# Kernel tuning notes

Hardware: AMD Instinct MI355X
Metric: run time of the kernel (lower is better)

Reference implementation:

```python
import jax, jax.numpy as jnp
import numpy as np

EMBED = 1024
HEADS = 16
HEAD_DIM = EMBED // HEADS
B, S = 2, 2048


def setup_inputs() -> dict:
    key = jax.random.key(0)
    ks = jax.random.split(key, 13)
    def lin(kw, kb):
        # torch nn.Linear default init: U(-1/sqrt(fan_in), 1/sqrt(fan_in))
        bound = 1.0 / np.sqrt(EMBED)
        W = jax.random.uniform(kw, (EMBED, EMBED), jnp.float32, -bound, bound)
        b = jax.random.uniform(kb, (EMBED,), jnp.float32, -bound, bound)
        return W, b
    Wq, bq = lin(ks[0], ks[1])
    Wk, bk = lin(ks[2], ks[3])
    Wv, bv = lin(ks[4], ks[5])
    Wo, bo = lin(ks[6], ks[7])
    return {
        "query": jax.random.normal(ks[8], (B, S, EMBED), jnp.float32),
        "key": jax.random.normal(ks[9], (B, S, EMBED), jnp.float32),
        "value": jax.random.normal(ks[10], (B, S, EMBED), jnp.float32),
        "mask": jax.random.randint(ks[11], (B, S, S), 0, 2, jnp.int32),
        "Wq": Wq, "bq": bq, "Wk": Wk, "bk": bk,
        "Wv": Wv, "bv": bv, "Wo": Wo, "bo": bo,
    }


def _split_heads(x):
    b, s, _ = x.shape
    return x.reshape(b, s, HEADS, HEAD_DIM).transpose(0, 2, 1, 3)  # [B,H,S,D]


def reference(query, key, value, mask, Wq, bq, Wk, bk, Wv, bv, Wo, bo):
    scaling = HEAD_DIM ** -0.5
    q = _split_heads(query @ Wq.T + bq) * scaling          # [B,H,Sq,D]
    k = _split_heads(key @ Wk.T + bk)                       # [B,H,Sk,D]
    v = _split_heads(value @ Wv.T + bv)                     # [B,H,Sk,D]
    scores = jnp.einsum('bhqd,bhkd->bhqk', q, k)            # [B,H,Sq,Sk]
    scores = jnp.where(mask[:, None, :, :] == 0, jnp.float32(-10000.0), scores)
    p = jax.nn.softmax(scores, axis=-1)
    x = jnp.einsum('bhqk,bhkd->bhqd', p, v)                 # [B,H,Sq,D]
    b, h, s, d = x.shape
    x = x.transpose(0, 2, 1, 3).reshape(b, s, h * d)
    return x @ Wo.T + bo
```

## Files before the change

kernel.cpp:

```cpp
#include <hip/hip_runtime.h>

#define EMBED 1024
#define HEADS 16
#define HDIM  64
#define BATCH 2
#define SEQ   2048
#define MTOT  (BATCH*SEQ)
#define LOG2E 1.4426950408889634f
#define QSCALE (0.125f * LOG2E)

typedef __attribute__((ext_vector_type(8)))  short short8;
typedef __attribute__((ext_vector_type(4)))  float f32x4;
typedef __attribute__((ext_vector_type(16))) float f32x16;

#define MFMA(a,b,c)   __builtin_amdgcn_mfma_f32_16x16x32_bf16(a,b,c,0,0,0)
#define MFMA32(a,b,c) __builtin_amdgcn_mfma_f32_32x32x16_bf16(a,b,c,0,0,0)

__device__ __forceinline__ ushort f2bf(float f) {
  union { float f; unsigned u; } v; v.f = f;
  unsigned u = v.u;
  unsigned r = u + 0x7fffu + ((u >> 16) & 1u);
  return (ushort)(r >> 16);
}
__device__ __forceinline__ unsigned packbf(float a, float b) {
  return (unsigned)f2bf(a) | ((unsigned)f2bf(b) << 16);
}
__device__ __forceinline__ unsigned cvtpk(float lo, float hi) {
  unsigned r;
  asm("v_cvt_pk_bf16_f32 %0, %1, %2" : "=v"(r) : "v"(lo), "v"(hi));
  return r;
}
__device__ __forceinline__ uint2 cvt4(float4 v) {
  uint2 r;
  asm("v_cvt_pk_bf16_f32 %0, %2, %3\n\t"
      "v_cvt_pk_bf16_f32 %1, %4, %5"
      : "=&v"(r.x), "=&v"(r.y)
      : "v"(v.x), "v"(v.y), "v"(v.z), "v"(v.w));
  return r;
}
__device__ __forceinline__ void gl_lds16(const ushort* g, ushort* l) {
  __builtin_amdgcn_global_load_lds(
      (const __attribute__((address_space(1))) unsigned*)g,
      (__attribute__((address_space(3))) unsigned*)l, 16, 0, 0);
}

__global__ __launch_bounds__(256) void tobf16(
    const float* __restrict__ s0, const float* __restrict__ s1, const float* __restrict__ s2,
    const float* __restrict__ s3, const float* __restrict__ s4, const float* __restrict__ s5,
    const float* __restrict__ s6,
    ushort* __restrict__ d0, ushort* __restrict__ d1, ushort* __restrict__ d2,
    ushort* __restrict__ d3, ushort* __restrict__ d4, ushort* __restrict__ d5,
    ushort* __restrict__ d6)
{
  const int z = blockIdx.z;
  const float* s; ushort* d;
  switch (z) {
    case 0: s = s0; d = d0; break;
    case 1: s = s1; d = d1; break;
    case 2: s = s2; d = d2; break;
    case 3: s = s3; d = d3; break;
    case 4: s = s4; d = d4; break;
    case 5: s = s5; d = d5; break;
    default: s = s6; d = d6; break;
  }
  const int nch = (z < 3) ? (MTOT * EMBED / 8) : (EMBED * EMBED / 8);
  int i = blockIdx.x * 256 + threadIdx.x;
  if (i >= nch) return;
  float4 a = reinterpret_cast<const float4*>(s)[2 * i];
  float4 b = reinterpret_cast<const float4*>(s)[2 * i + 1];
  uint2 lo = cvt4(a), hi = cvt4(b);
  reinterpret_cast<uint4*>(d)[i] = make_uint4(lo.x, lo.y, hi.x, hi.y);
}

__global__ __launch_bounds__(256) void maskpack(const int* __restrict__ mask,
                                                unsigned long long* __restrict__ bits) {
  size_t idx = (size_t)blockIdx.x * 256 + threadIdx.x;
  unsigned long long bal = __ballot(mask[idx] != 0);
  if ((threadIdx.x & 63) == 0) bits[idx >> 6] = bal;
}

__global__ __launch_bounds__(512, 6) void gemm_qkv32(
    const ushort* __restrict__ A0, const ushort* __restrict__ A1, const ushort* __restrict__ A2,
    const ushort* __restrict__ W0, const ushort* __restrict__ W1, const ushort* __restrict__ W2,
    const float* __restrict__ b0, const float* __restrict__ b1, const float* __restrict__ b2,
    ushort* __restrict__ oq, ushort* __restrict__ ok, ushort* __restrict__ ov)
{
  __shared__ __align__(16) ushort lds[2][2][4096];

  const int nwg = 768;
  int lin = blockIdx.x + (blockIdx.y << 3);
  int swz = (lin & 7) * (nwg >> 3) + (lin >> 3);
  const int z  = swz >> 8;
  const int r_ = swz & 255;
  const int n0 = (r_ & 7) << 7;
  const int m0 = (r_ >> 3) << 7;

  const ushort* __restrict__ A    = (z == 0) ? A0 : (z == 1) ? A1 : A2;
  const ushort* __restrict__ W    = (z == 0) ? W0 : (z == 1) ? W1 : W2;
  const float*  __restrict__ bias = (z == 0) ? b0 : (z == 1) ? b1 : b2;

  const int t = threadIdx.x;
  const int lane = t & 63;
  const int wid = t >> 6;
  const int wr = wid >> 2, wc = wid & 3;
  const int lr = lane & 15, qg = lane >> 4;

  const int srow = t >> 2;
  const int scol = ((((t & 3) - (srow >> 1)) & 3)) << 3;
  auto stage = [&](int buf, int k0) {
    gl_lds16(&A[(size_t)(m0 + srow) * EMBED + k0 + scol], &lds[buf][0][t * 8]);
    gl_lds16(&W[(size_t)(n0 + srow) * EMBED + k0 + scol], &lds[buf][1][t * 8]);
  };

  f32x4 acc[4][2] = {};

  stage(0, 0);
  asm volatile("s_waitcnt vmcnt(0)" ::: "memory");
  __syncthreads();

  for (int kt = 0; kt < 32; ++kt) {
    const int buf = kt & 1;
    if (kt < 31) stage(buf ^ 1, (kt + 1) * 32);

    short8 af[4], bfr[2];
    #pragma unroll
    for (int mi = 0; mi < 4; ++mi) {
      int row = wr * 64 + mi * 16 + lr;
      int sidx = (qg + (row >> 1)) & 3;
      af[mi] = *reinterpret_cast<const short8*>(&lds[buf][0][row * 32 + (sidx << 3)]);
    }
    #pragma unroll
    for (int ni = 0; ni < 2; ++ni) {
      int row = wc * 32 + ni * 16 + lr;
      int sidx = (qg + (row >> 1)) & 3;
      bfr[ni] = *reinterpret_cast<const short8*>(&lds[buf][1][row * 32 + (sidx << 3)]);
    }
    __builtin_amdgcn_s_setprio(1);
    #pragma unroll
    for (int mi = 0; mi < 4; ++mi)
      #pragma unroll
      for (int ni = 0; ni < 2; ++ni)
        acc[mi][ni] = MFMA(af[mi], bfr[ni], acc[mi][ni]);
    __builtin_amdgcn_s_setprio(0);

    if (kt < 31) {
      asm volatile("s_waitcnt vmcnt(0)" ::: "memory");
      __syncthreads();
    }
  }

  #pragma unroll
  for (int ni = 0; ni < 2; ++ni) {
    int ng = n0 + wc * 32 + ni * 16 + lr;
    float bv_ = bias[ng];
    int h = ng >> 6, d = ng & 63;
    #pragma unroll
    for (int mi = 0; mi < 4; ++mi) {
      #pragma unroll
      for (int r = 0; r < 4; ++r) {
        int mg = m0 + wr * 64 + mi * 16 + qg * 4 + r;
        float val = acc[mi][ni][r] + bv_;
        int bb = mg >> 11, s = mg & (SEQ - 1);
        int bh = bb * HEADS + h;
        if (z == 0)
          oq[((size_t)bh * SEQ + s) * HDIM + d] = f2bf(val * QSCALE);
        else if (z == 1)
          ok[((size_t)bh * SEQ + s) * HDIM + d] = f2bf(val);
        else {
          size_t addr = (((size_t)bh * 2 + (d >> 5)) * (SEQ / 32) + (s >> 5)) * 1024
                      + (size_t)(d & 31) * 32 + (s & 31);
          ov[addr] = f2bf(val);
        }
      }
    }
  }
}

__global__ __launch_bounds__(512, 4) void gemm_out128(
    const ushort* __restrict__ A0, const ushort* __restrict__ W0,
    const float* __restrict__ b0, float* __restrict__ of)
{
  __shared__ __align__(16) ushort lds[2][2][8192];

  const int nwg = 256;
  int lin = blockIdx.x + (blockIdx.y << 3);
  int swz = (lin & 7) * (nwg >> 3) + (lin >> 3);
  const int r_ = swz & 255;
  const int n0 = (r_ & 7) << 7;
  const int m0 = (r_ >> 3) << 7;

  const ushort* __restrict__ A = A0;
  const ushort* __restrict__ W = W0;
  const float*  __restrict__ bias = b0;

  const int t = threadIdx.x;
  const int lane = t & 63;
  const int wid = t >> 6;
  const int wr = wid >> 2, wc = wid & 3;
  const int lr = lane & 15, qg = lane >> 4;

  auto stage = [&](int buf, int k0) {
    #pragma unroll
    for (int it = 0; it < 2; ++it) {
      int idx = it * 512 + t;
      int row = idx >> 3;
      int col = ((idx & 7) ^ (row & 7)) << 3;
      gl_lds16(&A[(size_t)(m0 + row) * EMBED + k0 + col], &lds[buf][0][idx * 8]);
    }
    #pragma unroll
    for (int it = 0; it < 2; ++it) {
      int idx = it * 512 + t;
      int row = idx >> 3;
      int col = ((idx & 7) ^ (row & 7)) << 3;
      gl_lds16(&W[(size_t)(n0 + row) * EMBED + k0 + col], &lds[buf][1][idx * 8]);
    }
  };

  f32x4 acc[4][2] = {};

  stage(0, 0);
  asm volatile("s_waitcnt vmcnt(0)" ::: "memory");
  __syncthreads();

  for (int kt = 0; kt < 16; ++kt) {
    const int buf = kt & 1;
    if (kt < 15) stage(buf ^ 1, (kt + 1) * 64);

    #pragma unroll
    for (int ks = 0; ks < 2; ++ks) {
      short8 af[4], bfr[2];
      #pragma unroll
      for (int mi = 0; mi < 4; ++mi) {
        int row = wr * 64 + mi * 16 + lr;
        int cp = (ks * 4 + qg) ^ (row & 7);
        af[mi] = *reinterpret_cast<const short8*>(&lds[buf][0][row * 64 + (cp << 3)]);
      }
      #pragma unroll
      for (int ni = 0; ni < 2; ++ni) {
        int row = wc * 32 + ni * 16 + lr;
        int cp = (ks * 4 + qg) ^ (row & 7);
        bfr[ni] = *reinterpret_cast<const short8*>(&lds[buf][1][row * 64 + (cp << 3)]);
      }
      __builtin_amdgcn_s_setprio(1);
      #pragma unroll
      for (int mi = 0; mi < 4; ++mi)
        #pragma unroll
        for (int ni = 0; ni < 2; ++ni)
          acc[mi][ni] = MFMA(af[mi], bfr[ni], acc[mi][ni]);
      __builtin_amdgcn_s_setprio(0);
    }

    if (kt < 15) {
      asm volatile("s_waitcnt vmcnt(0)" ::: "memory");
      __syncthreads();
    }
  }

  #pragma unroll
  for (int ni = 0; ni < 2; ++ni) {
    int ng = n0 + wc * 32 + ni * 16 + lr;
    float bv_ = bias[ng];
    #pragma unroll
    for (int mi = 0; mi < 4; ++mi) {
      #pragma unroll
      for (int r = 0; r < 4; ++r) {
        int mg = m0 + wr * 64 + mi * 16 + qg * 4 + r;
        of[(size_t)mg * EMBED + ng] = acc[mi][ni][r] + bv_;
      }
    }
  }
}

__global__ __launch_bounds__(256, 2) void attn(
    const ushort* __restrict__ qws, const ushort* __restrict__ kws,
    const ushort* __restrict__ vws, const unsigned* __restrict__ mbits,
    ushort* __restrict__ xws)
{
  const int t = threadIdx.x;
  const int wid = t >> 6;
  const int l = t & 63;
  const int q31 = l & 31;
  const int h = l >> 5;

  const int L = blockIdx.x;
  const int j = L >> 3;
  const int bh = ((L & 7) << 2) + (j >> 4);
  const int q0 = (j & 15) << 7;
  const int b = bh >> 4, head = bh & 15;

  __shared__ __align__(16) ushort lds[9216];

  const int qrow = q0 + wid * 32 + q31;
  const ushort* qp = qws + ((size_t)bh * SEQ + qrow) * HDIM + 8 * h;
  short8 qf[4];
  #pragma unroll
  for (int s = 0; s < 4; ++s)
    qf[s] = *reinterpret_cast<const short8*>(qp + 16 * s);

  const int rp = (q31 & 19) | ((q31 & 4) << 1) | ((q31 & 8) >> 1);

  int koff[4];
  #pragma unroll
  for (int i = 0; i < 4; ++i)
    koff[i] = rp * 64 + (((h + 2 * i) ^ (rp & 7)) << 3);
  int voff[2][2];
  #pragma unroll
  for (int sb = 0; sb < 2; ++sb)
    #pragma unroll
    for (int jj = 0; jj < 2; ++jj)
      voff[sb][jj] = sb * 1024 + q31 * 32 + (((h + 2 * jj) ^ ((q31 >> 1) & 3)) << 3);

  const ushort* ksb = kws + (size_t)bh * SEQ * HDIM
                    + ((t >> 3) << 6) + (((t & 7) ^ ((t >> 3) & 7)) << 3);
  const int vsub = t >> 7, vd = (t >> 2) & 31, vc = t & 3;
  const ushort* vsb = vws + (((size_t)bh * 2 + vsub) << 16)
                    + vd * 32 + ((vc ^ ((vd >> 1) & 3)) << 3);
  ushort* kd0 = lds + t * 8;
  ushort* vd0 = lds + 2048 + t * 8;

  const unsigned* mp = mbits + (size_t)(b * SEQ + qrow) * (SEQ / 32);

  f32x16 accT[2] = {};
  float ls0 = 0.f, ls1 = 0.f, ls2 = 0.f, ls3 = 0.f;

  auto STAGE = [&](int tile, int bb) {
    gl_lds16(ksb + (size_t)tile * 2048, kd0 + bb);
    gl_lds16(vsb + (size_t)tile * 1024, vd0 + bb);
  };

  auto COMP = [&](int bb, unsigned mwc) {
    const ushort* kb = lds + bb;
    const ushort* vb = lds + bb + 2048;
    short8 kf0 = *reinterpret_cast<const short8*>(kb + koff[0]);
    short8 kf1 = *reinterpret_cast<const short8*>(kb + koff[1]);
    short8 kf2 = *reinterpret_cast<const short8*>(kb + koff[2]);
    short8 kf3 = *reinterpret_cast<const short8*>(kb + koff[3]);
    __builtin_amdgcn_s_setprio(1);
    f32x16 s = {};
    s = MFMA32(kf0, qf[0], s);
    s = MFMA32(kf1, qf[1], s);
    s = MFMA32(kf2, qf[2], s);
    s = MFMA32(kf3, qf[3], s);
    __builtin_amdgcn_s_setprio(0);

    short8 vf0 = *reinterpret_cast<const short8*>(vb + voff[0][0]);
    short8 vf1 = *reinterpret_cast<const short8*>(vb + voff[0][1]);
    short8 vf2 = *reinterpret_cast<const short8*>(vb + voff[1][0]);
    short8 vf3 = *reinterpret_cast<const short8*>(vb + voff[1][1]);

    unsigned msh = mwc >> (8 * h);
    union U { unsigned u[4]; short8 s8; } p0u, p1u;
    #pragma unroll
    for (int i = 0; i < 8; ++i) {
      const int r0 = 2 * i, r1 = 2 * i + 1;
      float e0 = ((msh >> ((r0 & 7) + 16 * (r0 >> 3))) & 1u) ? __builtin_amdgcn_exp2f(s[r0]) : 0.0f;
      float e1 = ((msh >> ((r1 & 7) + 16 * (r1 >> 3))) & 1u) ? __builtin_amdgcn_exp2f(s[r1]) : 0.0f;
      if ((i & 3) == 0) ls0 += e0 + e1;
      else if ((i & 3) == 1) ls1 += e0 + e1;
      else if ((i & 3) == 2) ls2 += e0 + e1;
      else ls3 += e0 + e1;
      if (i < 4) p0u.u[i] = cvtpk(e0, e1);
      else       p1u.u[i - 4] = cvtpk(e0, e1);
    }

    __builtin_amdgcn_s_setprio(1);
    accT[0] = MFMA32(vf0, p0u.s8, accT[0]);
    accT[0] = MFMA32(vf1, p1u.s8, accT[0]);
    accT[1] = MFMA32(vf2, p0u.s8, accT[1]);
    accT[1] = MFMA32(vf3, p1u.s8, accT[1]);
    __builtin_amdgcn_s_setprio(0);
  };

  unsigned mw = *mp; ++mp;
  STAGE(0, 0);
  asm volatile("s_waitcnt vmcnt(0)" ::: "memory");
  __syncthreads();

  #pragma unroll 1
  for (int it = 0; it < 32; ++it) {
    STAGE(2 * it + 1, 4096);
    unsigned mn = *mp; ++mp;
    COMP(0, mw);
    asm volatile("s_waitcnt vmcnt(0)" ::: "memory");
    __syncthreads();
    mw = mn;
    if (it < 31) STAGE(2 * it + 2, 0);
    mn = *mp; ++mp;
    COMP(4096, mw);
    asm volatile("s_waitcnt vmcnt(0)" ::: "memory");
    __syncthreads();
    mw = mn;
  }

  float lsum = (ls0 + ls1) + (ls2 + ls3);
  float lrow = lsum + __shfl_xor(lsum, 32);
  float inv = 1.0f / lrow;

  ushort* xb = lds + wid * 2304;
  #pragma unroll
  for (int nb = 0; nb < 2; ++nb)
    #pragma unroll
    for (int rg = 0; rg < 4; ++rg) {
      int dbase = 32 * nb + 8 * rg + 4 * h;
      uint2 pk = make_uint2(
          packbf(accT[nb][4 * rg] * inv,     accT[nb][4 * rg + 1] * inv),
          packbf(accT[nb][4 * rg + 2] * inv, accT[nb][4 * rg + 3] * inv));
      *reinterpret_cast<uint2*>(&xb[q31 * 72 + dbase]) = pk;
    }
  asm volatile("" ::: "memory");
  #pragma unroll
  for (int pp = 0; pp < 4; ++pp) {
    int row = pp * 8 + (l >> 3);
    int col = (l & 7) * 8;
    short8 xv = *reinterpret_cast<const short8*>(&xb[row * 72 + col]);
    *reinterpret_cast<short8*>(
        &xws[((size_t)b * SEQ + q0 + wid * 32 + row) * EMBED + head * HDIM + col]) = xv;
  }
}

extern "C" void kernel_launch(void* const* d_in, const int* in_sizes, int n_in,
                              void* d_out, int out_size, void* d_ws, size_t ws_size,
                              hipStream_t stream) {
  (void)in_sizes; (void)n_in; (void)out_size; (void)ws_size;
  const float* query = (const float*)d_in[0];
  const float* key   = (const float*)d_in[1];
  const float* value = (const float*)d_in[2];
  const int*   mask  = (const int*)d_in[3];
  const float* Wq = (const float*)d_in[4];  const float* bq = (const float*)d_in[5];
  const float* Wk = (const float*)d_in[6];  const float* bk = (const float*)d_in[7];
  const float* Wv = (const float*)d_in[8];  const float* bv = (const float*)d_in[9];
  const float* Wo = (const float*)d_in[10]; const float* bo = (const float*)d_in[11];
  float* out = (float*)d_out;

  const size_t NQKV = (size_t)BATCH * HEADS * SEQ * HDIM;
  const size_t NW   = (size_t)EMBED * EMBED;
  ushort* qws = (ushort*)d_ws;
  ushort* kws = qws + NQKV;
  ushort* vws = kws + NQKV;
  ushort* xws = vws + NQKV;
  unsigned* mbits = (unsigned*)(xws + NQKV);
  ushort* aqb = (ushort*)(mbits + (size_t)BATCH * SEQ * SEQ / 32);
  ushort* akb = aqb + NQKV;
  ushort* avb = akb + NQKV;
  ushort* wqb = avb + NQKV;
  ushort* wkb = wqb + NW;
  ushort* wvb = wkb + NW;
  ushort* wob = wvb + NW;

  tobf16<<<dim3((NQKV / 8 + 255) / 256, 1, 7), 256, 0, stream>>>(
      query, key, value, Wq, Wk, Wv, Wo, aqb, akb, avb, wqb, wkb, wvb, wob);

  maskpack<<<(BATCH * SEQ * SEQ) / 256, 256, 0, stream>>>(mask, (unsigned long long*)mbits);

  gemm_qkv32<<<dim3(8, 96), 512, 0, stream>>>(
      aqb, akb, avb, wqb, wkb, wvb, bq, bk, bv, qws, kws, vws);

  attn<<<dim3(512), 256, 0, stream>>>(qws, kws, vws, mbits, xws);

  gemm_out128<<<dim3(8, 32), 512, 0, stream>>>(xws, wob, bo, out);
}
```

Baseline: 150.7 us.

## Halve attention block size to 64 queries and compute row sums via MFMA

Attention blocks shrink from 4 waves (128 queries) to 2 waves (64 queries), and the grid doubles to 1024 blocks. Each thread now stages two K/V chunks into LDS so the tile loads stay the same. The softmax row sum is no longer accumulated with scalar adds and a cross-lane shuffle; it comes from extra MFMAs against a ones vector. This aims to improve occupancy and load balance and to take VALU work off the exp loop, at the cost of two more MFMAs per tile and less K/V reuse per block.

```diff
diff --git a/kernel.cpp b/kernel.cpp
--- a/kernel.cpp
+++ b/kernel.cpp
@@ -271,7 +271,7 @@
   }
 }
 
-__global__ __launch_bounds__(256, 2) void attn(
+__global__ __launch_bounds__(128) void attn(
     const ushort* __restrict__ qws, const ushort* __restrict__ kws,
     const ushort* __restrict__ vws, const unsigned* __restrict__ mbits,
     ushort* __restrict__ xws)
@@ -284,8 +284,8 @@
 
   const int L = blockIdx.x;
   const int j = L >> 3;
-  const int bh = ((L & 7) << 2) + (j >> 4);
-  const int q0 = (j & 15) << 7;
+  const int bh = ((L & 7) << 2) + (j >> 5);
+  const int q0 = (j & 31) << 6;
   const int b = bh >> 4, head = bh & 15;
 
   __shared__ __align__(16) ushort lds[9216];
@@ -310,22 +310,33 @@
     for (int jj = 0; jj < 2; ++jj)
       voff[sb][jj] = sb * 1024 + q31 * 32 + (((h + 2 * jj) ^ ((q31 >> 1) & 3)) << 3);
 
-  const ushort* ksb = kws + (size_t)bh * SEQ * HDIM
-                    + ((t >> 3) << 6) + (((t & 7) ^ ((t >> 3) & 7)) << 3);
-  const int vsub = t >> 7, vd = (t >> 2) & 31, vc = t & 3;
-  const ushort* vsb = vws + (((size_t)bh * 2 + vsub) << 16)
-                    + vd * 32 + ((vc ^ ((vd >> 1) & 3)) << 3);
-  ushort* kd0 = lds + t * 8;
-  ushort* vd0 = lds + 2048 + t * 8;
+  const ushort* ksb[2];
+  const ushort* vsb[2];
+  #pragma unroll
+  for (int it = 0; it < 2; ++it) {
+    int idx = it * 128 + t;
+    int krow = idx >> 3, kslot = idx & 7;
+    ksb[it] = kws + (size_t)bh * SEQ * HDIM + krow * 64 + ((kslot ^ (krow & 7)) << 3);
+    int vsub = idx >> 7, vd = (idx >> 2) & 31, vc = idx & 3;
+    vsb[it] = vws + (((size_t)bh * 2 + vsub) << 16) + vd * 32 + ((vc ^ ((vd >> 1) & 3)) << 3);
+  }
 
   const unsigned* mp = mbits + (size_t)(b * SEQ + qrow) * (SEQ / 32);
 
+  short8 onesf;
+  #pragma unroll
+  for (int i = 0; i < 8; ++i) onesf[i] = (short)0x3F80;
+
   f32x16 accT[2] = {};
-  float ls0 = 0.f, ls1 = 0.f, ls2 = 0.f, ls3 = 0.f;
+  f32x16 acc_l = {};
 
   auto STAGE = [&](int tile, int bb) {
-    gl_lds16(ksb + (size_t)tile * 2048, kd0 + bb);
-    gl_lds16(vsb + (size_t)tile * 1024, vd0 + bb);
+    #pragma unroll
+    for (int it = 0; it < 2; ++it) {
+      int idx = it * 128 + t;
+      gl_lds16(ksb[it] + (size_t)tile * 2048, lds + bb + idx * 8);
+      gl_lds16(vsb[it] + (size_t)tile * 1024, lds + bb + 2048 + idx * 8);
+    }
   };
 
   auto COMP = [&](int bb, unsigned mwc) {
@@ -355,10 +366,6 @@
       const int r0 = 2 * i, r1 = 2 * i + 1;
       float e0 = ((msh >> ((r0 & 7) + 16 * (r0 >> 3))) & 1u) ? __builtin_amdgcn_exp2f(s[r0]) : 0.0f;
       float e1 = ((msh >> ((r1 & 7) + 16 * (r1 >> 3))) & 1u) ? __builtin_amdgcn_exp2f(s[r1]) : 0.0f;
-      if ((i & 3) == 0) ls0 += e0 + e1;
-      else if ((i & 3) == 1) ls1 += e0 + e1;
-      else if ((i & 3) == 2) ls2 += e0 + e1;
-      else ls3 += e0 + e1;
       if (i < 4) p0u.u[i] = cvtpk(e0, e1);
       else       p1u.u[i - 4] = cvtpk(e0, e1);
     }
@@ -368,6 +375,8 @@
     accT[0] = MFMA32(vf1, p1u.s8, accT[0]);
     accT[1] = MFMA32(vf2, p0u.s8, accT[1]);
     accT[1] = MFMA32(vf3, p1u.s8, accT[1]);
+    acc_l   = MFMA32(onesf, p0u.s8, acc_l);
+    acc_l   = MFMA32(onesf, p1u.s8, acc_l);
     __builtin_amdgcn_s_setprio(0);
   };
 
@@ -392,8 +401,7 @@
     mw = mn;
   }
 
-  float lsum = (ls0 + ls1) + (ls2 + ls3);
-  float lrow = lsum + __shfl_xor(lsum, 32);
+  float lrow = acc_l[0];
   float inv = 1.0f / lrow;
 
   ushort* xb = lds + wid * 2304;
@@ -455,7 +463,7 @@
   gemm_qkv32<<<dim3(8, 96), 512, 0, stream>>>(
       aqb, akb, avb, wqb, wkb, wvb, bq, bk, bv, qws, kws, vws);
 
-  attn<<<dim3(512), 256, 0, stream>>>(qws, kws, vws, mbits, xws);
+  attn<<<dim3(1024), 128, 0, stream>>>(qws, kws, vws, mbits, xws);
 
   gemm_out128<<<dim3(8, 32), 512, 0, stream>>>(xws, wob, bo, out);
 }
```

Measured after the change: 161.3 us. 7.0% more time.

## Triple-buffer K/V tiles in attention loop with partial vmcnt waits

Applied to the files above, without the earlier changes.

Moves the attention K/V staging from a double buffer to a three-slot ring, prefetching two tiles ahead. Each iteration now waits only with vmcnt(2), so the next tile's loads can stay in flight across the barrier instead of draining every load. LDS use grows from 9216 to 12288 ushorts per block, which may limit occupancy. The vmcnt counting also has to stay correct alongside the per-iteration mask word loads.

```diff
diff --git a/kernel.cpp b/kernel.cpp
--- a/kernel.cpp
+++ b/kernel.cpp
@@ -288,7 +288,7 @@
   const int q0 = (j & 15) << 7;
   const int b = bh >> 4, head = bh & 15;
 
-  __shared__ __align__(16) ushort lds[9216];
+  __shared__ __align__(16) ushort lds[12288];
 
   const int qrow = q0 + wid * 32 + q31;
   const ushort* qp = qws + ((size_t)bh * SEQ + qrow) * HDIM + 8 * h;
@@ -315,17 +315,16 @@
   const int vsub = t >> 7, vd = (t >> 2) & 31, vc = t & 3;
   const ushort* vsb = vws + (((size_t)bh * 2 + vsub) << 16)
                     + vd * 32 + ((vc ^ ((vd >> 1) & 3)) << 3);
-  ushort* kd0 = lds + t * 8;
-  ushort* vd0 = lds + 2048 + t * 8;
 
   const unsigned* mp = mbits + (size_t)(b * SEQ + qrow) * (SEQ / 32);
 
   f32x16 accT[2] = {};
   float ls0 = 0.f, ls1 = 0.f, ls2 = 0.f, ls3 = 0.f;
 
-  auto STAGE = [&](int tile, int bb) {
-    gl_lds16(ksb + (size_t)tile * 2048, kd0 + bb);
-    gl_lds16(vsb + (size_t)tile * 1024, vd0 + bb);
+  auto STAGE = [&](int tile, int buf) {
+    ushort* base = lds + buf * 4096;
+    gl_lds16(ksb + (size_t)tile * 2048, base + t * 8);
+    gl_lds16(vsb + (size_t)tile * 1024, base + 2048 + t * 8);
   };
 
   auto COMP = [&](int bb, unsigned mwc) {
@@ -373,24 +372,26 @@
 
   unsigned mw = *mp; ++mp;
   STAGE(0, 0);
-  asm volatile("s_waitcnt vmcnt(0)" ::: "memory");
+  STAGE(1, 1);
+  asm volatile("s_waitcnt vmcnt(2)" ::: "memory");
+  __builtin_amdgcn_s_barrier();
+  asm volatile("" ::: "memory");
+
+  #pragma unroll 1
+  for (int tile = 0; tile < 64; ++tile) {
+    unsigned mn = 0;
+    if (tile < 63) { mn = *mp; ++mp; }
+    if (tile < 62) STAGE(tile + 2, (tile + 2) % 3);
+    COMP((tile % 3) * 4096, mw);
+    if (tile < 62)       asm volatile("s_waitcnt vmcnt(2)" ::: "memory");
+    else if (tile == 62) asm volatile("s_waitcnt vmcnt(0)" ::: "memory");
+    if (tile < 63) {
+      __builtin_amdgcn_s_barrier();
+      asm volatile("" ::: "memory");
+    }
+    mw = mn;
+  }
   __syncthreads();
-
-  #pragma unroll 1
-  for (int it = 0; it < 32; ++it) {
-    STAGE(2 * it + 1, 4096);
-    unsigned mn = *mp; ++mp;
-    COMP(0, mw);
-    asm volatile("s_waitcnt vmcnt(0)" ::: "memory");
-    __syncthreads();
-    mw = mn;
-    if (it < 31) STAGE(2 * it + 2, 0);
-    mn = *mp; ++mp;
-    COMP(4096, mw);
-    asm volatile("s_waitcnt vmcnt(0)" ::: "memory");
-    __syncthreads();
-    mw = mn;
-  }
 
   float lsum = (ls0 + ls1) + (ls2 + ls3);
   float lrow = lsum + __shfl_xor(lsum, 32);
```

New measurement: 162.0 us. +7.5%, slower.

## Process two key tiles per pipeline stage to halve barriers

Applied to the files above, without the earlier changes.

Each attention pipeline stage now loads and computes 64 keys instead of 32, with LDS doubled to hold two 32-key K/V tiles per buffer. The loop count drops from 32 to 16 iterations, so there are half as many waitcnt/barrier synchronizations, and each wave has more independent MFMA and softmax work to interleave. In exchange, LDS use rises to 32KB per block and register pressure grows from the extra fragments, which could hurt occupancy at launch bounds 2.

```diff
diff --git a/kernel.cpp b/kernel.cpp
--- a/kernel.cpp
+++ b/kernel.cpp
@@ -288,7 +288,7 @@
   const int q0 = (j & 15) << 7;
   const int b = bh >> 4, head = bh & 15;
 
-  __shared__ __align__(16) ushort lds[9216];
+  __shared__ __align__(16) ushort lds[16384];
 
   const int qrow = q0 + wid * 32 + q31;
   const ushort* qp = qws + ((size_t)bh * SEQ + qrow) * HDIM + 8 * h;
@@ -310,45 +310,33 @@
     for (int jj = 0; jj < 2; ++jj)
       voff[sb][jj] = sb * 1024 + q31 * 32 + (((h + 2 * jj) ^ ((q31 >> 1) & 3)) << 3);
 
-  const ushort* ksb = kws + (size_t)bh * SEQ * HDIM
-                    + ((t >> 3) << 6) + (((t & 7) ^ ((t >> 3) & 7)) << 3);
+  const ushort* ksb[2];
+  #pragma unroll
+  for (int it = 0; it < 2; ++it) {
+    int idx = it * 256 + t;
+    int krow = idx >> 3, kslot = idx & 7;
+    ksb[it] = kws + (size_t)bh * SEQ * HDIM + krow * 64 + ((kslot ^ (krow & 7)) << 3);
+  }
   const int vsub = t >> 7, vd = (t >> 2) & 31, vc = t & 3;
   const ushort* vsb = vws + (((size_t)bh * 2 + vsub) << 16)
                     + vd * 32 + ((vc ^ ((vd >> 1) & 3)) << 3);
-  ushort* kd0 = lds + t * 8;
-  ushort* vd0 = lds + 2048 + t * 8;
 
   const unsigned* mp = mbits + (size_t)(b * SEQ + qrow) * (SEQ / 32);
 
   f32x16 accT[2] = {};
   float ls0 = 0.f, ls1 = 0.f, ls2 = 0.f, ls3 = 0.f;
 
-  auto STAGE = [&](int tile, int bb) {
-    gl_lds16(ksb + (size_t)tile * 2048, kd0 + bb);
-    gl_lds16(vsb + (size_t)tile * 1024, vd0 + bb);
+  auto STAGE = [&](int step, int bb) {
+    ushort* base = lds + bb;
+    #pragma unroll
+    for (int it = 0; it < 2; ++it)
+      gl_lds16(ksb[it] + (size_t)step * 4096, base + (it * 256 + t) * 8);
+    gl_lds16(vsb + (size_t)(2 * step) * 1024,     base + 4096 + t * 8);
+    gl_lds16(vsb + (size_t)(2 * step + 1) * 1024, base + 6144 + t * 8);
   };
 
-  auto COMP = [&](int bb, unsigned mwc) {
-    const ushort* kb = lds + bb;
-    const ushort* vb = lds + bb + 2048;
-    short8 kf0 = *reinterpret_cast<const short8*>(kb + koff[0]);
-    short8 kf1 = *reinterpret_cast<const short8*>(kb + koff[1]);
-    short8 kf2 = *reinterpret_cast<const short8*>(kb + koff[2]);
-    short8 kf3 = *reinterpret_cast<const short8*>(kb + koff[3]);
-    __builtin_amdgcn_s_setprio(1);
-    f32x16 s = {};
-    s = MFMA32(kf0, qf[0], s);
-    s = MFMA32(kf1, qf[1], s);
-    s = MFMA32(kf2, qf[2], s);
-    s = MFMA32(kf3, qf[3], s);
-    __builtin_amdgcn_s_setprio(0);
-
-    short8 vf0 = *reinterpret_cast<const short8*>(vb + voff[0][0]);
-    short8 vf1 = *reinterpret_cast<const short8*>(vb + voff[0][1]);
-    short8 vf2 = *reinterpret_cast<const short8*>(vb + voff[1][0]);
-    short8 vf3 = *reinterpret_cast<const short8*>(vb + voff[1][1]);
-
-    unsigned msh = mwc >> (8 * h);
+  auto SOFTMAX16 = [&](const f32x16& s, unsigned msh,
+                       short8& pa, short8& pb) {
     union U { unsigned u[4]; short8 s8; } p0u, p1u;
     #pragma unroll
     for (int i = 0; i < 8; ++i) {
@@ -362,34 +350,76 @@
       if (i < 4) p0u.u[i] = cvtpk(e0, e1);
       else       p1u.u[i - 4] = cvtpk(e0, e1);
     }
-
+    pa = p0u.s8; pb = p1u.s8;
+  };
+
+  auto COMP = [&](int bb, unsigned mw0, unsigned mw1) {
+    const ushort* kb = lds + bb;
+    const ushort* vb = lds + bb + 4096;
+    short8 kfa0 = *reinterpret_cast<const short8*>(kb + koff[0]);
+    short8 kfa1 = *reinterpret_cast<const short8*>(kb + koff[1]);
+    short8 kfa2 = *reinterpret_cast<const short8*>(kb + koff[2]);
+    short8 kfa3 = *reinterpret_cast<const short8*>(kb + koff[3]);
+    short8 kfb0 = *reinterpret_cast<const short8*>(kb + koff[0] + 2048);
+    short8 kfb1 = *reinterpret_cast<const short8*>(kb + koff[1] + 2048);
+    short8 kfb2 = *reinterpret_cast<const short8*>(kb + koff[2] + 2048);
+    short8 kfb3 = *reinterpret_cast<const short8*>(kb + koff[3] + 2048);
     __builtin_amdgcn_s_setprio(1);
-    accT[0] = MFMA32(vf0, p0u.s8, accT[0]);
-    accT[0] = MFMA32(vf1, p1u.s8, accT[0]);
-    accT[1] = MFMA32(vf2, p0u.s8, accT[1]);
-    accT[1] = MFMA32(vf3, p1u.s8, accT[1]);
+    f32x16 sa = {}, sb = {};
+    sa = MFMA32(kfa0, qf[0], sa);
+    sa = MFMA32(kfa1, qf[1], sa);
+    sa = MFMA32(kfa2, qf[2], sa);
+    sa = MFMA32(kfa3, qf[3], sa);
+    sb = MFMA32(kfb0, qf[0], sb);
+    sb = MFMA32(kfb1, qf[1], sb);
+    sb = MFMA32(kfb2, qf[2], sb);
+    sb = MFMA32(kfb3, qf[3], sb);
+    __builtin_amdgcn_s_setprio(0);
+
+    short8 vf0a = *reinterpret_cast<const short8*>(vb + voff[0][0]);
+    short8 vf1a = *reinterpret_cast<const short8*>(vb + voff[0][1]);
+    short8 vf2a = *reinterpret_cast<const short8*>(vb + voff[1][0]);
+    short8 vf3a = *reinterpret_cast<const short8*>(vb + voff[1][1]);
+    short8 vf0b = *reinterpret_cast<const short8*>(vb + 2048 + voff[0][0]);
+    short8 vf1b = *reinterpret_cast<const short8*>(vb + 2048 + voff[0][1]);
+    short8 vf2b = *reinterpret_cast<const short8*>(vb + 2048 + voff[1][0]);
+    short8 vf3b = *reinterpret_cast<const short8*>(vb + 2048 + voff[1][1]);
+
+    short8 pa0, pa1, pb0, pb1;
+    SOFTMAX16(sa, mw0 >> (8 * h), pa0, pa1);
+    SOFTMAX16(sb, mw1 >> (8 * h), pb0, pb1);
+
+    __builtin_amdgcn_s_setprio(1);
+    accT[0] = MFMA32(vf0a, pa0, accT[0]);
+    accT[0] = MFMA32(vf1a, pa1, accT[0]);
+    accT[1] = MFMA32(vf2a, pa0, accT[1]);
+    accT[1] = MFMA32(vf3a, pa1, accT[1]);
+    accT[0] = MFMA32(vf0b, pb0, accT[0]);
+    accT[0] = MFMA32(vf1b, pb1, accT[0]);
+    accT[1] = MFMA32(vf2b, pb0, accT[1]);
+    accT[1] = MFMA32(vf3b, pb1, accT[1]);
     __builtin_amdgcn_s_setprio(0);
   };
 
-  unsigned mw = *mp; ++mp;
+  unsigned mw0 = mp[0], mw1 = mp[1]; mp += 2;
   STAGE(0, 0);
   asm volatile("s_waitcnt vmcnt(0)" ::: "memory");
   __syncthreads();
 
   #pragma unroll 1
-  for (int it = 0; it < 32; ++it) {
-    STAGE(2 * it + 1, 4096);
-    unsigned mn = *mp; ++mp;
-    COMP(0, mw);
+  for (int it = 0; it < 16; ++it) {
+    STAGE(2 * it + 1, 8192);
+    unsigned mn0 = mp[0], mn1 = mp[1]; mp += 2;
+    COMP(0, mw0, mw1);
     asm volatile("s_waitcnt vmcnt(0)" ::: "memory");
     __syncthreads();
-    mw = mn;
-    if (it < 31) STAGE(2 * it + 2, 0);
-    mn = *mp; ++mp;
-    COMP(4096, mw);
+    mw0 = mn0; mw1 = mn1;
+    if (it < 15) STAGE(2 * it + 2, 0);
+    mn0 = mp[0]; mn1 = mp[1]; mp += 2;
+    COMP(8192, mw0, mw1);
     asm volatile("s_waitcnt vmcnt(0)" ::: "memory");
     __syncthreads();
-    mw = mn;
+    mw0 = mn0; mw1 = mn1;
   }
 
   float lsum = (ls0 + ls1) + (ls2 + ls3);
```

Result: no change. 151.9 us (+0.8%).
